# Optimization experiments

Hardware: AMD Instinct MI355X
Metric: run time of the kernel (lower is better)

The kernel has to match this reference:

```python
import jax, jax.numpy as jnp
import numpy as np

NUM_HEADS = 32
HEAD_DIM = 128
ROPE_THETA = 10000.0


def _rope_tables(seq_len, head_dim, theta):
    inv_freq = 1.0 / (theta ** (jnp.arange(0, head_dim, 2, dtype=jnp.float32) / head_dim))
    pos = jnp.arange(seq_len, dtype=jnp.float32)
    freqs = pos[:, None] * inv_freq[None, :]            # [S, hd/2]
    emb = jnp.concatenate([freqs, freqs], axis=-1)      # [S, hd]
    return jnp.cos(emb), jnp.sin(emb)


def _rotate_half(x):
    x1, x2 = jnp.split(x, 2, axis=-1)
    return jnp.concatenate([-x2, x1], axis=-1)


def _apply_rope(x, cos, sin):
    # x: [B, S, H, D]; cos/sin: [S, D] -> unsqueeze_dim=2 broadcasting
    c = cos[None, :, None, :]
    s = sin[None, :, None, :]
    return x * c + _rotate_half(x) * s


def setup_inputs() -> dict:
    key = jax.random.key(0)
    ks = jax.random.split(key, 6)
    hidden = 4096
    B, S = 2, 4096  # global sequence = world_size * local_seq (4 * 1024)
    hidden_states = jax.random.normal(ks[0], (B, S, hidden), dtype=jnp.float32)
    # original uses torch.rand (uniform); scaled by 0.02 for numerical sanity
    q_proj = jax.random.uniform(ks[1], (hidden, hidden), dtype=jnp.float32) * 0.02
    k_proj = jax.random.uniform(ks[2], (hidden, hidden), dtype=jnp.float32) * 0.02
    v_proj = jax.random.uniform(ks[3], (hidden, hidden), dtype=jnp.float32) * 0.02
    o_proj = jax.random.uniform(ks[4], (hidden, hidden), dtype=jnp.float32) * 0.02
    return {"hidden_states": hidden_states, "q_proj": q_proj, "k_proj": k_proj,
            "v_proj": v_proj, "o_proj": o_proj, "world_size": 4}


def _ring_attention(hidden_states, q_proj, k_proj, v_proj, o_proj, world_size):
    B, S, H = hidden_states.shape
    s_local = S // world_size
    nh, hd = NUM_HEADS, HEAD_DIM
    scale = 1.0 / np.sqrt(hd).astype(np.float32)

    # rank 0 holds the first sequence shard as its local hidden states
    hs_local = hidden_states[:, :s_local]
    q = (hs_local @ q_proj.T).reshape(B, s_local, nh, hd)
    k = (hidden_states @ k_proj.T).reshape(B, S, nh, hd)
    v = (hidden_states @ v_proj.T).reshape(B, S, nh, hd)

    cos, sin = _rope_tables(S, hd, ROPE_THETA)
    q = _apply_rope(q, cos[:s_local], sin[:s_local])   # rank0 positions 0..s_local-1
    k = _apply_rope(k, cos, sin)                       # global positions per shard

    # split into per-rank KV blocks; rank 0 receives blocks W-1, W-2, ..., 0
    k_blocks = k.reshape(B, world_size, s_local, nh, hd).transpose(1, 0, 2, 3, 4)[::-1]
    v_blocks = v.reshape(B, world_size, s_local, nh, hd).transpose(1, 0, 2, 3, 4)[::-1]

    def step(carry, kv):
        attn, max_lse, denom, lse_full = carry
        k_blk, v_blk = kv
        # memory_efficient_attention_partial: non-causal partial attention + lse
        s = jnp.einsum('bqhd,bkhd->bhqk', q, k_blk) * scale
        m = jnp.max(s, axis=-1)                          # [B,H,q]
        p = jnp.exp(s - m[..., None])
        l = jnp.sum(p, axis=-1)
        lse = (m + jnp.log(l)).transpose(0, 2, 1)        # [B,q,H]
        out = jnp.einsum('bhqk,bkhd->bqhd', p / l[..., None], v_blk)
        # online-softmax merge across ring steps
        new_max = jnp.maximum(max_lse, lse)
        old_adj = jnp.exp(max_lse - new_max)[..., None]
        new_adj = jnp.exp(lse - new_max)[..., None]
        denom = old_adj * denom + new_adj
        attn = old_adj * attn + new_adj * out
        lse_full = new_max + jnp.log(jnp.exp(lse_full - new_max) + jnp.exp(lse - new_max))
        return (attn, new_max, denom, lse_full), None

    init = (jnp.zeros((B, s_local, nh, hd), jnp.float32),
            jnp.full((B, s_local, nh), -jnp.inf, jnp.float32),
            jnp.zeros((B, s_local, nh, 1), jnp.float32),
            jnp.full((B, s_local, nh), -jnp.inf, jnp.float32))
    (attn, _, denom, _), _ = jax.lax.scan(step, init, (k_blocks, v_blocks))

    attn = attn / denom
    attn = attn.astype(jnp.float16).astype(jnp.float32)  # .half() in source
    attn = attn.reshape(B, s_local, nh * hd)
    return attn @ o_proj.T


def reference(hidden_states, q_proj, k_proj, v_proj, o_proj, world_size):
    return _ring_attention(hidden_states, q_proj, k_proj, v_proj, o_proj, world_size)
```

## Files before the change

kernel.cpp:

```cpp
#include <hip/hip_runtime.h>
#include <hip/hip_bf16.h>


using bf16x8 = __attribute__((ext_vector_type(8))) short;
using f32x4  = __attribute__((ext_vector_type(4))) float;

__device__ inline unsigned short f32_to_bf16_bits(float f) {
  unsigned int u = __float_as_uint(f);
  u += 0x7FFFu + ((u >> 16) & 1u);
  return (unsigned short)(u >> 16);
}
__device__ inline float bf16_bits_to_f32(unsigned short h) {
  return __uint_as_float(((unsigned int)h) << 16);
}
__device__ inline unsigned short f32_to_bf16_fast(float f) {
  __hip_bfloat16 hb = __float2bfloat16(f);
  unsigned short us;
  __builtin_memcpy(&us, &hb, 2);
  return us;
}

__device__ __forceinline__ void load_lds16(const unsigned short* g, unsigned short* l) {
  __builtin_amdgcn_global_load_lds(
      (const __attribute__((address_space(1))) void*)g,
      (__attribute__((address_space(3))) void*)l, 16, 0, 0);
}

__global__ void cast_f32_bf16_batched(const float* __restrict__ hs,
                                      const float* __restrict__ w0,
                                      const float* __restrict__ w1,
                                      const float* __restrict__ w2,
                                      const float* __restrict__ w3,
                                      unsigned short* __restrict__ out) {
  const long hs4 = 2L * 4096 * 4096 / 4;
  const long w4  = 4096L * 4096 / 4;
  long i = (long)blockIdx.x * blockDim.x + threadIdx.x;
  long stride = (long)gridDim.x * blockDim.x;
  const long total = hs4 + 4 * w4;
  for (; i < total; i += stride) {
    const float* src;
    long j = i;
    if (j < hs4) { src = hs; }
    else {
      j -= hs4;
      long wi = j / w4;
      j -= wi * w4;
      src = (wi == 0) ? w0 : (wi == 1) ? w1 : (wi == 2) ? w2 : w3;
    }
    float4 v = reinterpret_cast<const float4*>(src)[j];
    ushort4 o;
    o.x = f32_to_bf16_bits(v.x);
    o.y = f32_to_bf16_bits(v.y);
    o.z = f32_to_bf16_bits(v.z);
    o.w = f32_to_bf16_bits(v.w);
    reinterpret_cast<ushort4*>(out)[i] = o;
  }
}

__global__ void rope_tables(float* __restrict__ cos_t, float* __restrict__ sin_t) {
  int idx = blockIdx.x * 256 + threadIdx.x;
  if (idx >= 4096 * 64) return;
  int p = idx >> 6, i = idx & 63;
  float inv = __expf(-(float)i * (9.210340371976184f / 64.0f));
  float f = (float)p * inv;
  cos_t[idx] = cosf(f);
  sin_t[idx] = sinf(f);
}

__global__ void rope_apply_qk(unsigned short* __restrict__ qbuf,
                              unsigned short* __restrict__ kbuf,
                              const float4* __restrict__ cos4,
                              const float4* __restrict__ sin4,
                              float qgain) {
  const long qch = 2048L * 256;
  const long kch = 8192L * 256;
  long idx = (long)blockIdx.x * 256 + threadIdx.x;
  if (idx >= qch + kch) return;
  unsigned short* buf;
  int pos_mask; float gain;
  if (idx < qch) { buf = qbuf; pos_mask = 1023; gain = qgain; }
  else { idx -= qch; buf = kbuf; pos_mask = 4095; gain = 1.0f; }
  long tok = idx >> 8;
  int rem = (int)(idx & 255);
  int head = rem >> 3, c = rem & 7;
  int pos = (int)(tok & (long)pos_mask);
  float4 ct0 = cos4[pos * 16 + c * 2];
  float4 ct1 = cos4[pos * 16 + c * 2 + 1];
  float4 st0 = sin4[pos * 16 + c * 2];
  float4 st1 = sin4[pos * 16 + c * 2 + 1];
  float cs[8] = {ct0.x, ct0.y, ct0.z, ct0.w, ct1.x, ct1.y, ct1.z, ct1.w};
  float sn[8] = {st0.x, st0.y, st0.z, st0.w, st1.x, st1.y, st1.z, st1.w};
  long base = tok * 4096 + head * 128 + c * 8;
  bf16x8 x1 = *reinterpret_cast<const bf16x8*>(buf + base);
  bf16x8 x2 = *reinterpret_cast<const bf16x8*>(buf + base + 64);
  bf16x8 o1, o2;
#pragma unroll
  for (int j = 0; j < 8; j++) {
    float a = bf16_bits_to_f32((unsigned short)x1[j]);
    float b = bf16_bits_to_f32((unsigned short)x2[j]);
    o1[j] = (short)f32_to_bf16_bits((a * cs[j] - b * sn[j]) * gain);
    o2[j] = (short)f32_to_bf16_bits((b * cs[j] + a * sn[j]) * gain);
  }
  *reinterpret_cast<bf16x8*>(buf + base) = o1;
  *reinterpret_cast<bf16x8*>(buf + base + 64) = o2;
}

__device__ inline void storeC(float* p, float v) { *p = v; }
__device__ inline void storeC(unsigned short* p, float v) { *p = f32_to_bf16_bits(v); }

template <typename OUT_T>
__global__ __launch_bounds__(256) void gemm_bt(const unsigned short* __restrict__ A,
                                               const unsigned short* __restrict__ B,
                                               OUT_T* __restrict__ C,
                                               long Astride_z, long Cstride_z, int N) {
  __shared__ unsigned short As[128 * 32];
  __shared__ unsigned short Bs[128 * 32];
  const int tid = threadIdx.x;
  const int bn = blockIdx.x, bm = blockIdx.y, bz = blockIdx.z;
  const unsigned short* Ab = A + (long)bz * Astride_z + (long)bm * 128 * 4096;
  const unsigned short* Bb = B + (long)bn * 128 * 4096;
  OUT_T* Cb = C + (long)bz * Cstride_z + (long)bm * 128 * N + (long)bn * 128;

  const int lane = tid & 63;
  const int w = tid >> 6;
  const int wr = (w >> 1) * 64, wc = (w & 1) * 64;
  const int fr = lane & 15, fg = lane >> 4;

  f32x4 acc[4][4] = {};

  const int c0 = tid, c1 = tid + 256;
  const int rA0 = c0 >> 2, kc0 = c0 & 3;
  const int rA1 = c1 >> 2, kc1 = c1 & 3;

  for (int k0 = 0; k0 < 4096; k0 += 32) {
    load_lds16(Ab + (long)rA0 * 4096 + k0 + kc0 * 8, As + c0 * 8);
    load_lds16(Ab + (long)rA1 * 4096 + k0 + kc1 * 8, As + c1 * 8);
    load_lds16(Bb + (long)rA0 * 4096 + k0 + kc0 * 8, Bs + c0 * 8);
    load_lds16(Bb + (long)rA1 * 4096 + k0 + kc1 * 8, Bs + c1 * 8);
    __syncthreads();
    bf16x8 af[4], bfv[4];
#pragma unroll
    for (int m = 0; m < 4; m++)
      af[m] = *reinterpret_cast<const bf16x8*>(As + (wr + m * 16 + fr) * 32 + fg * 8);
#pragma unroll
    for (int n = 0; n < 4; n++)
      bfv[n] = *reinterpret_cast<const bf16x8*>(Bs + (wc + n * 16 + fr) * 32 + fg * 8);
#pragma unroll
    for (int m = 0; m < 4; m++)
#pragma unroll
      for (int n = 0; n < 4; n++)
        acc[m][n] = __builtin_amdgcn_mfma_f32_16x16x32_bf16(af[m], bfv[n], acc[m][n], 0, 0, 0);
    __syncthreads();
  }
#pragma unroll
  for (int m = 0; m < 4; m++)
#pragma unroll
    for (int n = 0; n < 4; n++)
#pragma unroll
      for (int r = 0; r < 4; r++) {
        int row = wr + m * 16 + fg * 4 + r;
        int col = wc + n * 16 + fr;
        storeC(Cb + (long)row * N + col, acc[m][n][r]);
      }
}

#define STG2(Gb, Lb, h, kc)                                                    \
  load_lds16((Gb) + (long)((h) * 128 + srow) * 4096 + sslot * 8 + (kc),        \
             (Lb) + tid * 8);                                                  \
  load_lds16((Gb) + (long)((h) * 128 + 64 + srow) * 4096 + sslot * 8 + (kc),   \
             (Lb) + 4096 + tid * 8);

#define MFMAQ(MH, NH)                                                          \
  _Pragma("unroll") for (int mi = 0; mi < 4; ++mi)                             \
    _Pragma("unroll") for (int ni = 0; ni < 2; ++ni)                           \
      _Pragma("unroll") for (int kk = 0; kk < 2; ++kk)                         \
        acc[(MH) * 4 + mi][(NH) * 2 + ni] =                                    \
            __builtin_amdgcn_mfma_f32_16x16x32_bf16(                           \
                a[mi][kk], b[(NH) * 2 + ni][kk],                               \
                acc[(MH) * 4 + mi][(NH) * 2 + ni], 0, 0, 0);

#define TILE(P, KC, MODE)                                                      \
  {                                                                            \
    const unsigned short* Ar = lds + wm * 16384 + (P) * 8192;                  \
    const unsigned short* Br =                                                 \
        lds + 32768 + (wn >> 1) * 16384 + (P) * 8192 + (wn & 1) * 4096;        \
    _Pragma("unroll") for (int mf = 0; mf < 4; ++mf) {                         \
      a[mf][0] = *reinterpret_cast<const bf16x8*>(Ar + mf * 1024 + ao0);       \
      a[mf][1] = *reinterpret_cast<const bf16x8*>(Ar + mf * 1024 + ao1);       \
    }                                                                          \
    _Pragma("unroll") for (int nf = 0; nf < 2; ++nf) {                         \
      b[nf][0] = *reinterpret_cast<const bf16x8*>(Br + nf * 1024 + ao0);       \
      b[nf][1] = *reinterpret_cast<const bf16x8*>(Br + nf * 1024 + ao1);       \
    }                                                                          \
    __builtin_amdgcn_s_setprio(1);                                             \
    MFMAQ(0, 0);                                                               \
    __builtin_amdgcn_s_setprio(0);                                             \
    _Pragma("unroll") for (int nf = 2; nf < 4; ++nf) {                         \
      b[nf][0] = *reinterpret_cast<const bf16x8*>(Br + nf * 1024 + ao0);       \
      b[nf][1] = *reinterpret_cast<const bf16x8*>(Br + nf * 1024 + ao1);       \
    }                                                                          \
    __builtin_amdgcn_s_setprio(1);                                             \
    MFMAQ(0, 1);                                                               \
    __builtin_amdgcn_s_setprio(0);                                             \
    asm volatile("s_waitcnt lgkmcnt(0)" ::: "memory");                         \
    asm volatile("s_barrier" ::: "memory");            \
    if ((MODE) == 0) {                                                         \
      STG2(Bg, lds + 32768 + (P) * 8192, 0, KC);                               \
      STG2(Bg, lds + 49152 + (P) * 8192, 1, KC);                               \
    }                                                                          \
    _Pragma("unroll") for (int mf = 0; mf < 4; ++mf) {                         \
      a[mf][0] = *reinterpret_cast<const bf16x8*>(Ar + (4 + mf) * 1024 + ao0); \
      a[mf][1] = *reinterpret_cast<const bf16x8*>(Ar + (4 + mf) * 1024 + ao1); \
    }                                                                          \
    __builtin_amdgcn_s_setprio(1);                                             \
    MFMAQ(1, 0);                                                               \
    __builtin_amdgcn_s_setprio(0);                                             \
    asm volatile("s_waitcnt lgkmcnt(0)" ::: "memory");                         \
    asm volatile("s_barrier" ::: "memory");            \
    if ((MODE) == 0) {                                                         \
      STG2(Ag, lds + (P) * 8192, 0, KC);                                       \
      STG2(Ag, lds + 16384 + (P) * 8192, 1, KC);                               \
    }                                                                          \
    __builtin_amdgcn_s_setprio(1);                                             \
    MFMAQ(1, 1);                                                               \
    __builtin_amdgcn_s_setprio(0);                                             \
    if ((MODE) == 0) asm volatile("s_waitcnt vmcnt(8)" ::: "memory");          \
    if ((MODE) == 1) asm volatile("s_waitcnt vmcnt(0)" ::: "memory");          \
    asm volatile("s_barrier" ::: "memory");       \
  }

template <typename OUT_T>
__global__ __launch_bounds__(512, 2) void gemm256(const unsigned short* __restrict__ A,
                                                  const unsigned short* __restrict__ B,
                                                  OUT_T* __restrict__ C,
                                                  long Astride_z, long Cstride_z, int N) {
  __shared__ unsigned short lds[65536];
  const int tid = threadIdx.x;
  const int bn = blockIdx.x, bm = blockIdx.y, bz = blockIdx.z;
  const unsigned short* Ag = A + (long)bz * Astride_z + (long)bm * 256 * 4096;
  const unsigned short* Bg = B + (long)bn * 256 * 4096;

  const int w = tid >> 6, lane = tid & 63;
  const int wm = w >> 2, wn = w & 3;
  const int fr = lane & 15, fg = lane >> 4;
  const int ao0 = fr * 64 + ((fg ^ (fr & 7)) * 8);
  const int ao1 = fr * 64 + (((4 + fg) ^ (fr & 7)) * 8);
  const int srow = tid >> 3;
  const int sslot = (tid & 7) ^ (srow & 7);

  f32x4 acc[8][4] = {};
  bf16x8 a[4][2], b[4][2];

  STG2(Ag, lds + 0, 0, 0);     STG2(Ag, lds + 16384, 1, 0);
  STG2(Bg, lds + 32768, 0, 0); STG2(Bg, lds + 49152, 1, 0);
  STG2(Ag, lds + 8192, 0, 64);  STG2(Ag, lds + 24576, 1, 64);
  STG2(Bg, lds + 40960, 0, 64); STG2(Bg, lds + 57344, 1, 64);
  asm volatile("s_waitcnt vmcnt(8)" ::: "memory");
  asm volatile("s_barrier" ::: "memory");

  for (int ti = 0; ti < 31; ++ti) {
    TILE(0, (2 * ti + 2) * 64, 0);
    TILE(1, (2 * ti + 3) * 64, 0);
  }
  TILE(0, 0, 1);
  TILE(1, 0, 2);

  OUT_T* Cb = C + (long)bz * Cstride_z + ((long)bm * 256) * N + bn * 256;
#pragma unroll
  for (int mf = 0; mf < 8; ++mf)
#pragma unroll
    for (int nf = 0; nf < 4; ++nf)
#pragma unroll
      for (int rr = 0; rr < 4; ++rr) {
        int row = wm * 128 + mf * 16 + fg * 4 + rr;
        int col = wn * 64 + nf * 16 + fr;
        storeC(Cb + (long)row * N + col, acc[mf][nf][rr]);
      }
}

__global__ __launch_bounds__(256) void attn_fwd(const unsigned short* __restrict__ qb,
                                                const unsigned short* __restrict__ kb,
                                                const unsigned short* __restrict__ vT,
                                                unsigned short* __restrict__ ob) {
  __shared__ unsigned short Ks[2][64 * 128];
  __shared__ unsigned short Vl[2][128 * 64];
  __shared__ unsigned short Ps[4][16 * 72];

  const int qt = blockIdx.x, h = blockIdx.y, b = blockIdx.z;
  const int tid = threadIdx.x, w = tid >> 6, lane = tid & 63;
  const int fr = lane & 15, fg = lane >> 4;

  const unsigned short* kbase = kb + (long)b * 4096 * 4096 + h * 128;
  const unsigned short* vbase = vT + (long)h * 128 * 8192 + (long)b * 4096;

  const unsigned short* kp[4];
  const unsigned short* vp[4];
  unsigned short* kl[4];
  unsigned short* vl[4];
#pragma unroll
  for (int i = 0; i < 4; i++) {
    int c = tid + 256 * i;
    int key = c >> 4, s0 = c & 15;
    kp[i] = kbase + (long)(64 + key) * 4096 + (s0 ^ (key & 15)) * 8;
    kl[i] = (unsigned short*)&Ks[0][c * 8];
    int f0 = c >> 3, s1 = c & 7;
    vp[i] = vbase + (long)f0 * 8192 + 64 + (s1 ^ (f0 & 7)) * 8;
    vl[i] = (unsigned short*)&Vl[0][c * 8];
  }
  const int pbytes = 64 * 128;

  bf16x8 qf[4];
  {
    const unsigned short* qptr =
        qb + ((long)b * 1024 + qt * 64 + w * 16 + fr) * 4096 + h * 128 + fg * 8;
#pragma unroll
    for (int c = 0; c < 4; c++) qf[c] = *reinterpret_cast<const bf16x8*>(qptr + c * 32);
  }

  f32x4 outa[8] = {};
  float m_run[4], l_run[4];
#pragma unroll
  for (int r = 0; r < 4; r++) { m_run[r] = -1e30f; l_run[r] = 0.0f; }

#pragma unroll
  for (int i = 0; i < 4; i++) {
    int c = tid + 256 * i;
    int key = c >> 4, s0 = c & 15;
    load_lds16(kbase + (long)key * 4096 + (s0 ^ (key & 15)) * 8, &Ks[0][c * 8]);
    int f0 = c >> 3, s1 = c & 7;
    load_lds16(vbase + (long)f0 * 8192 + (s1 ^ (f0 & 7)) * 8, &Vl[0][c * 8]);
  }
  asm volatile("s_waitcnt vmcnt(0)" ::: "memory");
  asm volatile("s_barrier" ::: "memory");

  for (int t = 0; t < 64; ++t) {
    const int cur = t & 1;
    if (t < 63) {
      const int po = (cur ^ 1) * pbytes;
#pragma unroll
      for (int i = 0; i < 4; i++) {
        load_lds16(kp[i], kl[i] + po);
        kp[i] += 64 * 4096;
        load_lds16(vp[i], vl[i] + po);
        vp[i] += 64;
      }
    }

    f32x4 sacc[4];
    __builtin_amdgcn_s_setprio(1);
#pragma unroll
    for (int ks = 0; ks < 4; ks++) {
      f32x4 aq = {0.f, 0.f, 0.f, 0.f};
#pragma unroll
      for (int cc = 0; cc < 4; cc++) {
        bf16x8 kf = *reinterpret_cast<const bf16x8*>(
            &Ks[cur][(ks * 16 + fr) * 128 + (((cc * 4 + fg) ^ fr) & 15) * 8]);
        aq = __builtin_amdgcn_mfma_f32_16x16x32_bf16(qf[cc], kf, aq, 0, 0, 0);
      }
      sacc[ks] = aq;
    }
    __builtin_amdgcn_s_setprio(0);

    float mxl[4];
    int need = 0;
#pragma unroll
    for (int r = 0; r < 4; r++) {
      mxl[r] = fmaxf(fmaxf(sacc[0][r], sacc[1][r]), fmaxf(sacc[2][r], sacc[3][r]));
      need |= (mxl[r] > m_run[r] + 11.5f) ? 1 : 0;
    }
    if (__any(need)) {
#pragma unroll
      for (int r = 0; r < 4; r++) {
        float mx = mxl[r];
        mx = fmaxf(mx, __shfl_xor(mx, 1));
        mx = fmaxf(mx, __shfl_xor(mx, 2));
        mx = fmaxf(mx, __shfl_xor(mx, 4));
        mx = fmaxf(mx, __shfl_xor(mx, 8));
        float mnew = fmaxf(m_run[r], mx);
        float ef = exp2f(m_run[r] - mnew);
        l_run[r] *= ef;
        m_run[r] = mnew;
#pragma unroll
        for (int ds = 0; ds < 8; ds++) outa[ds][r] *= ef;
      }
    }
#pragma unroll
    for (int r = 0; r < 4; r++) {
      float sum = 0.f;
#pragma unroll
      for (int ks = 0; ks < 4; ks++) {
        float pv = exp2f(sacc[ks][r] - m_run[r]);
        Ps[w][(fg * 4 + r) * 72 + ks * 16 + fr] = f32_to_bf16_fast(pv);
        sum += pv;
      }
      l_run[r] += sum;
    }

    __builtin_amdgcn_s_setprio(1);
#pragma unroll
    for (int c2 = 0; c2 < 2; c2++) {
      bf16x8 pf = *reinterpret_cast<const bf16x8*>(&Ps[w][fr * 72 + c2 * 32 + fg * 8]);
#pragma unroll
      for (int ds = 0; ds < 8; ds++) {
        int feat = ds * 16 + fr;
        int pch = ((c2 * 4 + fg) ^ (feat & 7)) & 7;
        bf16x8 vf = *reinterpret_cast<const bf16x8*>(&Vl[cur][feat * 64 + pch * 8]);
        outa[ds] = __builtin_amdgcn_mfma_f32_16x16x32_bf16(pf, vf, outa[ds], 0, 0, 0);
      }
    }
    __builtin_amdgcn_s_setprio(0);

    if (t < 63) {
      asm volatile("s_waitcnt vmcnt(0) lgkmcnt(0)" ::: "memory");
      asm volatile("s_barrier" ::: "memory");
    }
  }

#pragma unroll
  for (int r = 0; r < 4; r++) {
    float l = l_run[r];
    l += __shfl_xor(l, 1);
    l += __shfl_xor(l, 2);
    l += __shfl_xor(l, 4);
    l += __shfl_xor(l, 8);
    float inv = 1.0f / l;
    unsigned short* op =
        ob + ((long)b * 1024 + qt * 64 + w * 16 + fg * 4 + r) * 4096 + h * 128;
#pragma unroll
    for (int ds = 0; ds < 8; ds++) op[ds * 16 + fr] = f32_to_bf16_bits(outa[ds][r] * inv);
  }
}

extern "C" void kernel_launch(void* const* d_in, const int* in_sizes, int n_in,
                              void* d_out, int out_size, void* d_ws, size_t ws_size,
                              hipStream_t stream) {
  const float* hs = (const float*)d_in[0];
  const float* wq = (const float*)d_in[1];
  const float* wk = (const float*)d_in[2];
  const float* wv = (const float*)d_in[3];
  const float* wo = (const float*)d_in[4];
  float* out = (float*)d_out;

  const long hsN = 2L * 4096 * 4096;
  const long wN  = 4096L * 4096;

  unsigned short* hs_b = (unsigned short*)d_ws;
  unsigned short* wq_b = hs_b + hsN;
  unsigned short* wk_b = wq_b + wN;
  unsigned short* wv_b = wk_b + wN;
  unsigned short* wo_b = wv_b + wN;
  unsigned short* q_b  = wo_b + wN;
  unsigned short* k_b  = q_b + 2048L * 4096;
  unsigned short* vT_b = k_b + 8192L * 4096;
  unsigned short* at_b = vT_b + 8192L * 4096;
  float* cos_t = (float*)(at_b + 2048L * 4096);
  float* sin_t = cos_t + 4096 * 64;

  cast_f32_bf16_batched<<<dim3(8192), dim3(256), 0, stream>>>(
      hs, wq, wk, wv, wo, hs_b);

  rope_tables<<<dim3(1024), dim3(256), 0, stream>>>(cos_t, sin_t);

  gemm_bt<unsigned short><<<dim3(32, 8, 2), dim3(256), 0, stream>>>(
      hs_b, wq_b, q_b, 4096L * 4096, 1024L * 4096, 4096);
  gemm256<unsigned short><<<dim3(16, 16, 2), dim3(512), 0, stream>>>(
      hs_b, wk_b, k_b, 4096L * 4096, 4096L * 4096, 4096);
  gemm256<unsigned short><<<dim3(32, 16, 1), dim3(512), 0, stream>>>(
      wv_b, hs_b, vT_b, 0L, 0L, 8192);

  const float qgain = 0.08838834764831845f * 1.4426950408889634f;
  rope_apply_qk<<<dim3(10240), dim3(256), 0, stream>>>(
      q_b, k_b, (const float4*)cos_t, (const float4*)sin_t, qgain);

  attn_fwd<<<dim3(16, 32, 2), dim3(256), 0, stream>>>(q_b, k_b, vT_b, at_b);

  gemm_bt<float><<<dim3(32, 16, 1), dim3(256), 0, stream>>>(
      at_b, wo_b, out, 0L, 0L, 4096);
}
```

Baseline: 1.022 ms.

## Use 256-tile GEMM for Q and O projections and remap attention blocks per XCD

Replaces the simple 128x128 single-buffered gemm_bt kernel with the existing 256-tile gemm256 kernel for the Q projection and the output projection. This gives more data reuse per block and likely better pipelining. The attention launch becomes a flat 1D grid whose block index is remapped so that all query tiles of one (batch, head) pair land on the same XCD, which should improve L2 reuse of K/V. Fewer blocks on the smaller GEMMs (128 for the Q and O projections) may underfill the GPU.

```diff
diff --git a/kernel.cpp b/kernel.cpp
--- a/kernel.cpp
+++ b/kernel.cpp
@@ -108,62 +108,6 @@
 __device__ inline void storeC(float* p, float v) { *p = v; }
 __device__ inline void storeC(unsigned short* p, float v) { *p = f32_to_bf16_bits(v); }
 
-template <typename OUT_T>
-__global__ __launch_bounds__(256) void gemm_bt(const unsigned short* __restrict__ A,
-                                               const unsigned short* __restrict__ B,
-                                               OUT_T* __restrict__ C,
-                                               long Astride_z, long Cstride_z, int N) {
-  __shared__ unsigned short As[128 * 32];
-  __shared__ unsigned short Bs[128 * 32];
-  const int tid = threadIdx.x;
-  const int bn = blockIdx.x, bm = blockIdx.y, bz = blockIdx.z;
-  const unsigned short* Ab = A + (long)bz * Astride_z + (long)bm * 128 * 4096;
-  const unsigned short* Bb = B + (long)bn * 128 * 4096;
-  OUT_T* Cb = C + (long)bz * Cstride_z + (long)bm * 128 * N + (long)bn * 128;
-
-  const int lane = tid & 63;
-  const int w = tid >> 6;
-  const int wr = (w >> 1) * 64, wc = (w & 1) * 64;
-  const int fr = lane & 15, fg = lane >> 4;
-
-  f32x4 acc[4][4] = {};
-
-  const int c0 = tid, c1 = tid + 256;
-  const int rA0 = c0 >> 2, kc0 = c0 & 3;
-  const int rA1 = c1 >> 2, kc1 = c1 & 3;
-
-  for (int k0 = 0; k0 < 4096; k0 += 32) {
-    load_lds16(Ab + (long)rA0 * 4096 + k0 + kc0 * 8, As + c0 * 8);
-    load_lds16(Ab + (long)rA1 * 4096 + k0 + kc1 * 8, As + c1 * 8);
-    load_lds16(Bb + (long)rA0 * 4096 + k0 + kc0 * 8, Bs + c0 * 8);
-    load_lds16(Bb + (long)rA1 * 4096 + k0 + kc1 * 8, Bs + c1 * 8);
-    __syncthreads();
-    bf16x8 af[4], bfv[4];
-#pragma unroll
-    for (int m = 0; m < 4; m++)
-      af[m] = *reinterpret_cast<const bf16x8*>(As + (wr + m * 16 + fr) * 32 + fg * 8);
-#pragma unroll
-    for (int n = 0; n < 4; n++)
-      bfv[n] = *reinterpret_cast<const bf16x8*>(Bs + (wc + n * 16 + fr) * 32 + fg * 8);
-#pragma unroll
-    for (int m = 0; m < 4; m++)
-#pragma unroll
-      for (int n = 0; n < 4; n++)
-        acc[m][n] = __builtin_amdgcn_mfma_f32_16x16x32_bf16(af[m], bfv[n], acc[m][n], 0, 0, 0);
-    __syncthreads();
-  }
-#pragma unroll
-  for (int m = 0; m < 4; m++)
-#pragma unroll
-    for (int n = 0; n < 4; n++)
-#pragma unroll
-      for (int r = 0; r < 4; r++) {
-        int row = wr + m * 16 + fg * 4 + r;
-        int col = wc + n * 16 + fr;
-        storeC(Cb + (long)row * N + col, acc[m][n][r]);
-      }
-}
-
 #define STG2(Gb, Lb, h, kc)                                                    \
   load_lds16((Gb) + (long)((h) * 128 + srow) * 4096 + sslot * 8 + (kc),        \
              (Lb) + tid * 8);                                                  \
@@ -286,7 +230,12 @@
   __shared__ unsigned short Vl[2][128 * 64];
   __shared__ unsigned short Ps[4][16 * 72];
 
-  const int qt = blockIdx.x, h = blockIdx.y, b = blockIdx.z;
+  const int id = blockIdx.x;
+  const int xcd = id & 7, j = id >> 3;
+  const int hb = xcd + 8 * (j >> 4);
+  const int qt = j & 15;
+  const int h = hb & 31, b = hb >> 5;
+
   const int tid = threadIdx.x, w = tid >> 6, lane = tid & 63;
   const int fr = lane & 15, fg = lane >> 4;
 
@@ -307,7 +256,7 @@
     vp[i] = vbase + (long)f0 * 8192 + 64 + (s1 ^ (f0 & 7)) * 8;
     vl[i] = (unsigned short*)&Vl[0][c * 8];
   }
-  const int pbytes = 64 * 128;
+  const int pelem = 64 * 128;
 
   bf16x8 qf[4];
   {
@@ -336,7 +285,7 @@
   for (int t = 0; t < 64; ++t) {
     const int cur = t & 1;
     if (t < 63) {
-      const int po = (cur ^ 1) * pbytes;
+      const int po = (cur ^ 1) * pelem;
 #pragma unroll
       for (int i = 0; i < 4; i++) {
         load_lds16(kp[i], kl[i] + po);
@@ -461,7 +410,7 @@
 
   rope_tables<<<dim3(1024), dim3(256), 0, stream>>>(cos_t, sin_t);
 
-  gemm_bt<unsigned short><<<dim3(32, 8, 2), dim3(256), 0, stream>>>(
+  gemm256<unsigned short><<<dim3(16, 4, 2), dim3(512), 0, stream>>>(
       hs_b, wq_b, q_b, 4096L * 4096, 1024L * 4096, 4096);
   gemm256<unsigned short><<<dim3(16, 16, 2), dim3(512), 0, stream>>>(
       hs_b, wk_b, k_b, 4096L * 4096, 4096L * 4096, 4096);
@@ -472,8 +421,8 @@
   rope_apply_qk<<<dim3(10240), dim3(256), 0, stream>>>(
       q_b, k_b, (const float4*)cos_t, (const float4*)sin_t, qgain);
 
-  attn_fwd<<<dim3(16, 32, 2), dim3(256), 0, stream>>>(q_b, k_b, vT_b, at_b);
-
-  gemm_bt<float><<<dim3(32, 16, 1), dim3(256), 0, stream>>>(
+  attn_fwd<<<dim3(1024), dim3(256), 0, stream>>>(q_b, k_b, vT_b, at_b);
+
+  gemm256<float><<<dim3(16, 8, 1), dim3(512), 0, stream>>>(
       at_b, wo_b, out, 0L, 0L, 4096);
 }
```

Result: no change. 1.011 ms (-1.1%).
